# Kernel optimization log

Hardware: AMD Instinct MI355X
Metric: run time of the kernel (lower is better)

The kernel has to match this reference:

```python
import jax, jax.numpy as jnp
import numpy as np

EM_DIM = 64
GROUP = 16
DIM_IN = 1024


def _position_embedding(boxes, part_boxes):
    # boxes: [N,4], part_boxes: [P,4] -> [N,P,EM_DIM]
    xmin, ymin, xmax, ymax = [boxes[:, i:i + 1] for i in range(4)]            # [N,1]
    pxmin, pymin, pxmax, pymax = [part_boxes[:, i:i + 1].T for i in range(4)]  # [1,P]
    bw = xmax - xmin + 1.0
    bh = ymax - ymin + 1.0
    pw = pxmax - pxmin + 1.0
    ph = pymax - pymin + 1.0
    cx = 0.5 * (xmin + xmax)
    cy = 0.5 * (ymin + ymax)
    pcx = 0.5 * (pxmin + pxmax)
    pcy = 0.5 * (pymin + pymax)
    dx = jnp.abs((cx - pcx) / bw)
    dy = jnp.abs((cy - pcy) / bh)
    dx = jnp.log(jnp.where(dx < 1e-3, 1e-3, dx))
    dy = jnp.log(jnp.where(dy < 1e-3, 1e-3, dy))
    dw = jnp.log(pw / bw)
    dh = jnp.log(ph / bh)
    pos = jnp.stack([dx, dy, dw, dh], axis=2)                                  # [N,P,4]
    em_range = jnp.arange(EM_DIM // 8, dtype=pos.dtype) / (EM_DIM // 8)        # [8]
    em_mat = jnp.power(jnp.asarray(1000.0, pos.dtype), em_range)               # [8]
    div = (100.0 * pos)[..., None] / em_mat                                    # [N,P,4,8]
    emb = jnp.concatenate([jnp.sin(div), jnp.cos(div)], axis=3)                # [N,P,4,16]
    return emb.reshape(pos.shape[0], pos.shape[1], EM_DIM)


def _single_relation(boxes, part_boxes, bf, pf, Wg_w, Wg_b, Wq_w, Wq_b, Wk_w, Wk_b, conv_w, conv_b):
    N = bf.shape[0]
    P = pf.shape[0]
    emb = _position_embedding(boxes, part_boxes)                               # [N,P,64]
    pos_feat = jax.nn.relu(emb @ Wg_w.T + Wg_b)                                # [N,P,G]
    att_weight = jnp.transpose(pos_feat, (0, 2, 1))                            # [N,G,P]
    q = (bf @ Wq_w.T + Wq_b).reshape(N, GROUP, EM_DIM)                         # [N,G,64]
    k = (pf @ Wk_w.T + Wk_b).reshape(P, GROUP, EM_DIM)                         # [P,G,64]
    att = jnp.einsum('ngd,pgd->ngp', q, k) * (1.0 / GROUP)                     # [N,G,P]
    att_weight = jnp.where(att_weight < 1e-6, 1e-6, att_weight)
    sm = jax.nn.softmax(jnp.log(att_weight) + att, axis=2)                     # [N,G,P]
    out = jnp.einsum('ngp,pc->ngc', sm, pf)                                    # [N,G,dim_in]
    # grouped 1x1 conv: group g maps dim_in channels -> EM_DIM channels
    w3 = conv_w.reshape(GROUP, EM_DIM, DIM_IN)
    rel = jnp.einsum('ngc,goc->ngo', out, w3).reshape(N, GROUP * EM_DIM) + conv_b
    return rel                                                                  # [N, G*EM_DIM]


def setup_inputs() -> dict:
    key = jax.random.key(0)
    ks = jax.random.split(key, 12)
    N_TOT, P_TOT = 2048, 2048

    def make_rois(k1, k2, n, n1):
        xy = jax.random.uniform(k1, (n, 2), jnp.float32) * 800.0
        wh = jax.random.uniform(k2, (n, 2), jnp.float32) * 200.0 + 16.0
        boxes = jnp.concatenate([xy, xy + wh], axis=1)
        idx = jnp.concatenate([jnp.zeros((n1, 1)), jnp.ones((n - n1, 1))], axis=0).astype(jnp.float32)
        return jnp.concatenate([idx, boxes], axis=1)

    rois = make_rois(ks[0], ks[1], N_TOT, 1024)
    part_rois = make_rois(ks[2], ks[3], P_TOT, 1024)
    box_feats = jax.random.normal(ks[4], (N_TOT, DIM_IN), jnp.float32)
    part_feats = jax.random.normal(ks[5], (P_TOT, DIM_IN), jnp.float32)
    xav_g = float(np.sqrt(6.0 / (EM_DIM + GROUP)))
    xav_qk = float(np.sqrt(6.0 / (DIM_IN + GROUP * EM_DIM)))
    Wg_w = jax.random.uniform(ks[6], (GROUP, EM_DIM), jnp.float32, -xav_g, xav_g)
    Wg_b = jnp.zeros((GROUP,), jnp.float32)
    Wq_w = jax.random.uniform(ks[7], (GROUP * EM_DIM, DIM_IN), jnp.float32, -xav_qk, xav_qk)
    Wq_b = jnp.zeros((GROUP * EM_DIM,), jnp.float32)
    Wk_w = jax.random.uniform(ks[8], (GROUP * EM_DIM, DIM_IN), jnp.float32, -xav_qk, xav_qk)
    Wk_b = jnp.zeros((GROUP * EM_DIM,), jnp.float32)
    conv_w = jax.random.normal(ks[9], (GROUP * EM_DIM, DIM_IN), jnp.float32) * 0.02
    conv_b = jnp.zeros((GROUP * EM_DIM,), jnp.float32)
    return {"rois": rois, "part_rois": part_rois, "box_feats": box_feats,
            "part_feats": part_feats, "Wg_w": Wg_w, "Wg_b": Wg_b,
            "Wq_w": Wq_w, "Wq_b": Wq_b, "Wk_w": Wk_w, "Wk_b": Wk_b,
            "conv_w": conv_w, "conv_b": conv_b, "n1_boxes": 1024, "n1_parts": 1024}


def reference(rois, part_rois, box_feats, part_feats, Wg_w, Wg_b, Wq_w, Wq_b,
              Wk_w, Wk_b, conv_w, conv_b, n1_boxes, n1_parts):
    boxes = rois[:, 1:5]
    part_boxes = part_rois[:, 1:5]
    params = (Wg_w, Wg_b, Wq_w, Wq_b, Wk_w, Wk_b, conv_w, conv_b)
    rel1 = _single_relation(boxes[:n1_boxes], part_boxes[:n1_parts],
                            box_feats[:n1_boxes], part_feats[:n1_parts], *params)
    rel2 = _single_relation(boxes[n1_boxes:], part_boxes[n1_parts:],
                            box_feats[n1_boxes:], part_feats[n1_parts:], *params)
    return jnp.concatenate([rel1, rel2], axis=0)  # [N_total, GROUP*EM_DIM]
```

## Files before the change

kernel.cpp:

```cpp
#include <hip/hip_runtime.h>

typedef unsigned short u16;
using short8  = __attribute__((ext_vector_type(8))) short;
using float4v = __attribute__((ext_vector_type(4))) float;

__device__ __forceinline__ u16 f2bf(float f) {
    union { float f; unsigned u; } v; v.f = f;
    unsigned r = (v.u + 0x7fff + ((v.u >> 16) & 1)) >> 16;
    return (u16)r;
}
__device__ __forceinline__ float bf2f(u16 h) {
    union { unsigned u; float f; } v; v.u = ((unsigned)h) << 16; return v.f;
}
__device__ __forceinline__ unsigned pkbf(float lo, float hi) {
    unsigned d;
    asm("v_cvt_pk_bf16_f32 %0, %1, %2" : "=v"(d) : "v"(lo), "v"(hi));
    return d;
}
__device__ __forceinline__ float sin_rev(float r) {
    float f, s;
    asm("v_fract_f32 %0, %1" : "=v"(f) : "v"(r));
    asm("v_sin_f32 %0, %1" : "=v"(s) : "v"(f));
    return s;
}
__device__ __forceinline__ void dma16(const void* g, void* l) {
    __builtin_amdgcn_global_load_lds((const __attribute__((address_space(1))) void*)g,
                                     (__attribute__((address_space(3))) void*)l, 16, 0, 0);
}

__device__ __forceinline__ void cvt4(const float* __restrict__ s, u16* __restrict__ o, int i) {
    float4 v = ((const float4*)s)[i];
    uint2 r; r.x = pkbf(v.x, v.y); r.y = pkbf(v.z, v.w);
    ((uint2*)o)[i] = r;
}

__global__ __launch_bounds__(256)
void cvt_all(const float* __restrict__ s0, const float* __restrict__ s1,
             const float* __restrict__ s2, const float* __restrict__ s3,
             const float* __restrict__ s4, const float* __restrict__ prois,
             u16* __restrict__ o0, u16* __restrict__ o1, u16* __restrict__ o2,
             u16* __restrict__ o3, u16* __restrict__ o4, float4* __restrict__ PD,
             int na4, int nb4, int nw4, int PT) {
    int i = blockIdx.x * 256 + threadIdx.x;
    if (i < na4) { cvt4(s0, o0, i); return; }
    i -= na4;
    if (i < nb4) { cvt4(s1, o1, i); return; }
    i -= nb4;
    if (i < nw4) { cvt4(s2, o2, i); return; }
    i -= nw4;
    if (i < nw4) { cvt4(s3, o3, i); return; }
    i -= nw4;
    if (i < nw4) { cvt4(s4, o4, i); return; }
    i -= nw4;
    if (i < PT) {
        const float* pr = prois + (size_t)i * 5;
        float pxmin = pr[1], pymin = pr[2], pxmax = pr[3], pymax = pr[4];
        PD[i] = make_float4(0.5f * (pxmin + pxmax), 0.5f * (pymin + pymax),
                            __logf(pxmax - pxmin + 1.0f), __logf(pymax - pymin + 1.0f));
    }
}

__global__ __launch_bounds__(256)
void proj_posw(const u16* __restrict__ Ab, const u16* __restrict__ Pb,
               const u16* __restrict__ Wqb, const u16* __restrict__ Wkb,
               const u16* __restrict__ Cwb, const float* __restrict__ bq,
               const float* __restrict__ bk, u16* __restrict__ Qb,
               u16* __restrict__ Kb, u16* __restrict__ PVt,
               const float* __restrict__ rois, const float4* __restrict__ PD,
               const float* __restrict__ Wg_w, const float* __restrict__ Wg_b,
               u16* __restrict__ POSW, const int* __restrict__ n1b_p,
               const int* __restrict__ n1p_p, int PT) {
    __shared__ __align__(16) u16 SH[20992];

    const int grp = blockIdx.x / 11, rem = blockIdx.x % 11;
    const int t = threadIdx.x;
    const int w = t >> 6, lane = t & 63;
    const int fm = lane & 15, quad = lane >> 4;

    if (rem < 3) {
        u16* As = SH;
        u16* Ws = SH + 8192;
        u16* Tr = SH + 12288;
        const int pb = grp * 3 + rem;
        const int z = pb >> 8;
        const int m0 = ((pb >> 4) & 15) * 128, j0 = (pb & 15) * 64;
        const u16* A = (z == 0) ? Ab : Pb;
        const u16* W = (z == 0) ? Wqb : (z == 1 ? Wkb : Cwb);
        const int wm = w >> 1, wn = w & 1;
        const int lr = lane >> 3, lc = lane & 7, gch = lc ^ lr;

        float4v zero4 = {0.f, 0.f, 0.f, 0.f};
        float4v acc[4][2];
#pragma unroll
        for (int i = 0; i < 4; ++i) { acc[i][0] = zero4; acc[i][1] = zero4; }

        for (int k0 = 0; k0 < 1024; k0 += 64) {
#pragma unroll
            for (int i = 0; i < 4; ++i) {
                int row = w * 32 + i * 8 + lr;
                dma16(A + (size_t)(m0 + row) * 1024 + k0 + gch * 8,
                      As + (w * 32 + i * 8) * 64 + lane * 8);
            }
#pragma unroll
            for (int i = 0; i < 2; ++i) {
                int row = w * 16 + i * 8 + lr;
                dma16(W + (size_t)(j0 + row) * 1024 + k0 + gch * 8,
                      Ws + (w * 16 + i * 8) * 64 + lane * 8);
            }
            __syncthreads();
#pragma unroll
            for (int ks = 0; ks < 2; ++ks) {
                int c = ks * 4 + quad;
                short8 af[4], bf[2];
#pragma unroll
                for (int i = 0; i < 4; ++i) {
                    int ra = wm * 64 + i * 16 + fm;
                    af[i] = *(const short8*)(As + ra * 64 + ((c ^ (ra & 7)) * 8));
                }
#pragma unroll
                for (int j = 0; j < 2; ++j) {
                    int rb = wn * 32 + j * 16 + fm;
                    bf[j] = *(const short8*)(Ws + rb * 64 + ((c ^ (rb & 7)) * 8));
                }
#pragma unroll
                for (int i = 0; i < 4; ++i)
#pragma unroll
                    for (int j = 0; j < 2; ++j)
                        acc[i][j] = __builtin_amdgcn_mfma_f32_16x16x32_bf16(af[i], bf[j], acc[i][j], 0, 0, 0);
            }
            __syncthreads();
        }

        if (z < 2) {
            u16* O = z ? Kb : Qb;
            const float* bias = z ? bk : bq;
#pragma unroll
            for (int j = 0; j < 2; ++j) {
                int jl = wn * 32 + j * 16 + fm;
                float bb = bias[j0 + jl];
#pragma unroll
                for (int i = 0; i < 4; ++i) {
                    int mlb = wm * 64 + i * 16 + quad * 4;
#pragma unroll
                    for (int r = 0; r < 4; ++r)
                        Tr[(mlb + r) * 68 + jl] = f2bf(acc[i][j][r] + bb);
                }
            }
            __syncthreads();
#pragma unroll
            for (int i2 = 0; i2 < 4; ++i2) {
                int f = i2 * 2048 + t * 8;
                int ml = f >> 6, jl = f & 63;
                union { uint2 u2[2]; short8 s8; } uu;
                uu.u2[0] = *(const uint2*)(Tr + ml * 68 + jl);
                uu.u2[1] = *(const uint2*)(Tr + ml * 68 + jl + 4);
                *(short8*)(O + (size_t)(m0 + ml) * 1024 + j0 + jl) = uu.s8;
            }
        } else {
#pragma unroll
            for (int j = 0; j < 2; ++j) {
                int jl = wn * 32 + j * 16 + fm;
#pragma unroll
                for (int i = 0; i < 4; ++i) {
                    int mlb = wm * 64 + i * 16 + quad * 4;
                    uint2 pk;
                    pk.x = pkbf(acc[i][j][0], acc[i][j][1]);
                    pk.y = pkbf(acc[i][j][2], acc[i][j][3]);
                    *(uint2*)(Tr + jl * 136 + mlb) = pk;
                }
            }
            __syncthreads();
#pragma unroll
            for (int i2 = 0; i2 < 4; ++i2) {
                int f = i2 * 2048 + t * 8;
                int jl = f >> 7, ml = f & 127;
                union { uint2 u2[2]; short8 s8; } uu;
                uu.u2[0] = *(const uint2*)(Tr + jl * 136 + ml);
                uu.u2[1] = *(const uint2*)(Tr + jl * 136 + ml + 4);
                *(short8*)(PVt + (size_t)(j0 + jl) * PT + m0 + ml) = uu.s8;
            }
        }
        return;
    }

    u16* Wl = SH + w * 4224;

    const int n = grp * 8 + (rem - 3);
    const int n1b = *n1b_p, n1p = *n1p_p;
    const int hh = (n >= n1b) ? 1 : 0;
    const int p0 = hh ? n1p : 0;
    const int Ph = hh ? (PT - n1p) : n1p;

    float xmin = rois[n * 5 + 1], ymin = rois[n * 5 + 2];
    float xmax = rois[n * 5 + 3], ymax = rois[n * 5 + 4];
    float bw = xmax - xmin + 1.0f, bh = ymax - ymin + 1.0f;
    float cx = 0.5f * (xmin + xmax), cy = 0.5f * (ymin + ymax);

    const int jA = quad >> 1, trig = quad & 1;
    float cA   = (jA == 0) ? cx : cy;
    float invA = (jA == 0) ? (1.0f / bw) : (1.0f / bh);
    float lB   = (jA == 0) ? __logf(bw) : __logf(bh);
    float toff = trig ? 0.25f : 0.0f;

    const int g_ = fm;
    short8 b1, b2;
    {
        const float* w1 = Wg_w + g_ * 64 + quad * 8;
        const float* w2 = Wg_w + g_ * 64 + 32 + quad * 8;
        unsigned* p1 = (unsigned*)&b1;
        unsigned* p2 = (unsigned*)&b2;
#pragma unroll
        for (int kk = 0; kk < 4; ++kk) {
            p1[kk] = pkbf(w1[2 * kk], w1[2 * kk + 1]);
            p2[kk] = pkbf(w2[2 * kk], w2[2 * kk + 1]);
        }
    }
    float wgb = Wg_b[g_];

    const float inv_em[8] = {1.0f, 0.4216965034f, 0.1778279410f, 0.0749894209f,
                             0.0316227766f, 0.0133352143f, 0.0056234133f, 0.0023713737f};
    const float REV = 15.91549431f;
    const int prange = Ph >> 2;
    const int pb0 = w * prange;

    float4 pd_c = PD[p0 + pb0 + fm];

#pragma unroll 2
    for (int pt = 0; pt < 16; ++pt) {
        float4 pd_n;
        if (pt < 15) pd_n = PD[p0 + pb0 + pt * 16 + 16 + fm];
        float pc = (jA == 0) ? pd_c.x : pd_c.y;
        float lp = (jA == 0) ? pd_c.z : pd_c.w;
        float posA = __logf(fmaxf(fabsf(cA - pc) * invA, 0.001f));
        float posB = lp - lB;
        float br1 = posA * REV, br2 = posB * REV;
        float e1[8], e2[8];
#pragma unroll
        for (int k = 0; k < 8; ++k) {
            e1[k] = sin_rev(fmaf(br1, inv_em[k], toff));
            e2[k] = sin_rev(fmaf(br2, inv_em[k], toff));
        }
        short8 a1, a2;
        unsigned* pa1 = (unsigned*)&a1;
        unsigned* pa2 = (unsigned*)&a2;
#pragma unroll
        for (int kk = 0; kk < 4; ++kk) {
            pa1[kk] = pkbf(e1[2 * kk], e1[2 * kk + 1]);
            pa2[kk] = pkbf(e2[2 * kk], e2[2 * kk + 1]);
        }
        float4v acc = {wgb, wgb, wgb, wgb};
        acc = __builtin_amdgcn_mfma_f32_16x16x32_bf16(a1, b1, acc, 0, 0, 0);
        acc = __builtin_amdgcn_mfma_f32_16x16x32_bf16(a2, b2, acc, 0, 0, 0);

        float w0  = fmaxf(acc[0], 1e-6f);
        float w1v = fmaxf(acc[1], 1e-6f);
        float w2v = fmaxf(acc[2], 1e-6f);
        float w3v = fmaxf(acc[3], 1e-6f);
        uint2 wp; wp.x = pkbf(w0, w1v); wp.y = pkbf(w2v, w3v);
        *(uint2*)(Wl + pt * 264 + lane * 4) = wp;

        pd_c = pd_n;
    }

    const int p8 = (lane & 31) * 8;
    const int halfg = lane >> 5;
    const int itq = p8 >> 4;
    const int q0 = (p8 >> 2) & 3;
#pragma unroll
    for (int s = 0; s < 8; ++s) {
        int gg = s * 2 + halfg;
        union { uint2 u2[2]; short8 s8; } uu;
        uu.u2[0] = *(const uint2*)(Wl + itq * 264 + (q0 * 16 + gg) * 4);
        uu.u2[1] = *(const uint2*)(Wl + itq * 264 + ((q0 + 1) * 16 + gg) * 4);
        *(short8*)(POSW + ((size_t)n * 16 + gg) * 1024 + pb0 + p8) = uu.s8;
    }
}

__global__ __launch_bounds__(256)
void fused_rel(const u16* __restrict__ Qb, const u16* __restrict__ Kb,
               const u16* __restrict__ POSW, const u16* __restrict__ PVt,
               const float* __restrict__ conv_b, float* __restrict__ OUT,
               const int* __restrict__ n1b_p, const int* __restrict__ n1p_p, int PT) {
    __shared__ __align__(16) u16 Qs[64 * 64];
    __shared__ __align__(16) u16 Ks[2][64 * 64];
    __shared__ __align__(16) u16 Ps[2][64 * 64];
    __shared__ __align__(16) u16 Vs[2][64 * 64];
    __shared__ __align__(16) u16 Wt[4][16 * 64];

    const int n0 = blockIdx.x * 64, g = blockIdx.y;
    const int n1b = *n1b_p, n1p = *n1p_p;
    const int hh = (n0 >= n1b) ? 1 : 0;
    const int p0 = hh ? n1p : 0;
    const int Ph = hh ? (PT - n1p) : n1p;
    const int t = threadIdx.x;
    const int w = t >> 6, lane = t & 63;
    const int lr = lane >> 3, lc = lane & 7, gch = lc ^ lr;
    const int fm = lane & 15, quad = lane >> 4;
    const int swz = fm & 7;

    auto stage = [&](int pt, int buf) {
#pragma unroll
        for (int i = 0; i < 2; ++i) {
            int row = w * 16 + i * 8 + lr;
            dma16(Kb + (size_t)(p0 + pt * 64 + row) * 1024 + g * 64 + gch * 8,
                  Ks[buf] + (w * 16 + i * 8) * 64 + lane * 8);
            dma16(POSW + ((size_t)(n0 + row) * 16 + g) * 1024 + pt * 64 + gch * 8,
                  Ps[buf] + (w * 16 + i * 8) * 64 + lane * 8);
            dma16(PVt + (size_t)(g * 64 + row) * PT + p0 + pt * 64 + gch * 8,
                  Vs[buf] + (w * 16 + i * 8) * 64 + lane * 8);
        }
    };

    stage(0, 0);
#pragma unroll
    for (int i = 0; i < 2; ++i) {
        int row = w * 16 + i * 8 + lr;
        dma16(Qb + (size_t)(n0 + row) * 1024 + g * 64 + gch * 8,
              Qs + (w * 16 + i * 8) * 64 + lane * 8);
    }

    float4v zero4 = {0.f, 0.f, 0.f, 0.f};
    float4v oacc[4];
#pragma unroll
    for (int ob = 0; ob < 4; ++ob) oacc[ob] = zero4;
    float rsum = 0.0f;

    __syncthreads();

    const int nloc = w * 16 + fm;
    short8 qf[2];
#pragma unroll
    for (int kd = 0; kd < 2; ++kd) {
        int c = kd * 4 + quad;
        qf[kd] = *(const short8*)(Qs + nloc * 64 + ((c ^ swz) * 8));
    }
    u16* wrow = Wt[w] + fm * 64;

    const int NPT = Ph >> 6;
    for (int pt = 0; pt < NPT; ++pt) {
        int cur = pt & 1;
        if (pt + 1 < NPT) stage(pt + 1, cur ^ 1);
        const u16* ks_ = Ks[cur];
        const u16* ps_ = Ps[cur];
        const u16* vs_ = Vs[cur];

        float4v atc[4];
#pragma unroll
        for (int pi = 0; pi < 4; ++pi) atc[pi] = zero4;
#pragma unroll
        for (int kd = 0; kd < 2; ++kd) {
            int c = kd * 4 + quad;
#pragma unroll
            for (int pi = 0; pi < 4; ++pi) {
                int rp = pi * 16 + fm;
                short8 kf = *(const short8*)(ks_ + rp * 64 + ((c ^ swz) * 8));
                atc[pi] = __builtin_amdgcn_mfma_f32_16x16x32_bf16(kf, qf[kd], atc[pi], 0, 0, 0);
            }
        }

#pragma unroll
        for (int pi = 0; pi < 4; ++pi) {
            int co = ((pi * 2 + (quad >> 1)) ^ swz) * 8 + (quad & 1) * 4;
            uint2 pwp = *(const uint2*)(ps_ + nloc * 64 + co);
            const u16* pww = (const u16*)&pwp;
            float wv0 = bf2f(pww[0]) * __expf(atc[pi][0] * 0.0625f);
            float wv1 = bf2f(pww[1]) * __expf(atc[pi][1] * 0.0625f);
            float wv2 = bf2f(pww[2]) * __expf(atc[pi][2] * 0.0625f);
            float wv3 = bf2f(pww[3]) * __expf(atc[pi][3] * 0.0625f);
            rsum += (wv0 + wv1) + (wv2 + wv3);
            uint2 wp; wp.x = pkbf(wv0, wv1); wp.y = pkbf(wv2, wv3);
            *(uint2*)(wrow + co) = wp;
        }

#pragma unroll
        for (int m = 0; m < 2; ++m) {
            short8 af = *(const short8*)(wrow + (((m * 4 + quad) ^ swz) * 8));
#pragma unroll
            for (int ob = 0; ob < 4; ++ob) {
                int ro = ob * 16 + fm;
                short8 vf = *(const short8*)(vs_ + ro * 64 + (((m * 4 + quad) ^ swz) * 8));
                oacc[ob] = __builtin_amdgcn_mfma_f32_16x16x32_bf16(af, vf, oacc[ob], 0, 0, 0);
            }
        }

        __syncthreads();
    }

    float s = rsum;
    s += __shfl_xor(s, 16, 64);
    s += __shfl_xor(s, 32, 64);
    float inv[4];
#pragma unroll
    for (int r = 0; r < 4; ++r)
        inv[r] = 1.0f / __shfl(s, quad * 4 + r, 64);

    float bb[4];
#pragma unroll
    for (int ob = 0; ob < 4; ++ob) bb[ob] = conv_b[g * 64 + ob * 16 + fm];
#pragma unroll
    for (int ob = 0; ob < 4; ++ob)
#pragma unroll
        for (int r = 0; r < 4; ++r) {
            int nn = n0 + w * 16 + quad * 4 + r;
            OUT[(size_t)nn * 1024 + g * 64 + ob * 16 + fm] = oacc[ob][r] * inv[r] + bb[ob];
        }
}

extern "C" void kernel_launch(void* const* d_in, const int* in_sizes, int n_in,
                              void* d_out, int out_size, void* d_ws, size_t ws_size,
                              hipStream_t stream) {
    const float* rois   = (const float*)d_in[0];
    const float* prois  = (const float*)d_in[1];
    const float* bfeat  = (const float*)d_in[2];
    const float* pfeat  = (const float*)d_in[3];
    const float* Wg_w   = (const float*)d_in[4];
    const float* Wg_b   = (const float*)d_in[5];
    const float* Wq_w   = (const float*)d_in[6];
    const float* Wq_b   = (const float*)d_in[7];
    const float* Wk_w   = (const float*)d_in[8];
    const float* Wk_b   = (const float*)d_in[9];
    const float* conv_w = (const float*)d_in[10];
    const float* conv_b = (const float*)d_in[11];
    const int*   n1b    = (const int*)d_in[12];
    const int*   n1p    = (const int*)d_in[13];

    const int NT = in_sizes[2] / 1024;
    const int PT = in_sizes[3] / 1024;

    u16* Qb   = (u16*)d_ws;
    u16* Kb   = Qb + (size_t)NT * 1024;
    u16* PVt  = Kb + (size_t)PT * 1024;
    float4* PD = (float4*)(PVt + (size_t)1024 * PT);
    u16* POSW = (u16*)(PD + PT);
    u16* Ab   = POSW + (size_t)NT * 16 * 1024;
    u16* Pb   = Ab + (size_t)NT * 1024;
    u16* Wqb  = Pb + (size_t)PT * 1024;
    u16* Wkb  = Wqb + 1024 * 1024;
    u16* Cwb  = Wkb + 1024 * 1024;

    dim3 blk(256);
    int nf4 = NT * 1024 / 4, pf4 = PT * 1024 / 4, wf4 = 1024 * 1024 / 4;
    int tot = nf4 + pf4 + 3 * wf4 + PT;
    cvt_all<<<dim3((tot + 255) / 256), blk, 0, stream>>>(
        bfeat, pfeat, Wq_w, Wk_w, conv_w, prois, Ab, Pb, Wqb, Wkb, Cwb, PD,
        nf4, pf4, wf4, PT);

    proj_posw<<<dim3(256 * 11), blk, 0, stream>>>(Ab, Pb, Wqb, Wkb, Cwb,
                                                  Wq_b, Wk_b, Qb, Kb, PVt,
                                                  rois, PD, Wg_w, Wg_b, POSW,
                                                  n1b, n1p, PT);
    fused_rel<<<dim3(NT / 64, 16), blk, 0, stream>>>(Qb, Kb, POSW, PVt, conv_b,
                                                     (float*)d_out, n1b, n1p, PT);
}
```

Before: 173.8 us.

## Precompute part-box sin/cos tables and use angle-subtraction for width/height embedding

The dw/dh embedding term, log(pw)-log(bw), is separable. The per-part sin/cos of log(pw) are now computed once per part in the conversion kernel and stored in a table. Each pos-weight block combines them with per-box sin/cos through the angle-difference identity, replacing 8 hardware sin evaluations per iteration with table loads and FMAs. The pos-weight tile is also staged in two halves, which roughly halves shared memory (the GEMM transpose buffer now aliases the A buffer) to allow more resident blocks. The cost is extra global reads of the trig table and a small change in numerics.

```diff
diff --git a/kernel.cpp b/kernel.cpp
--- a/kernel.cpp
+++ b/kernel.cpp
@@ -27,6 +27,8 @@
     __builtin_amdgcn_global_load_lds((const __attribute__((address_space(1))) void*)g,
                                      (__attribute__((address_space(3))) void*)l, 16, 0, 0);
 }
+
+#define REVC 15.91549431f
 
 __device__ __forceinline__ void cvt4(const float* __restrict__ s, u16* __restrict__ o, int i) {
     float4 v = ((const float4*)s)[i];
@@ -40,7 +42,7 @@
              const float* __restrict__ s4, const float* __restrict__ prois,
              u16* __restrict__ o0, u16* __restrict__ o1, u16* __restrict__ o2,
              u16* __restrict__ o3, u16* __restrict__ o4, float4* __restrict__ PD,
-             int na4, int nb4, int nw4, int PT) {
+             float* __restrict__ PTRIG, int na4, int nb4, int nw4, int PT) {
     int i = blockIdx.x * 256 + threadIdx.x;
     if (i < na4) { cvt4(s0, o0, i); return; }
     i -= na4;
@@ -53,10 +55,22 @@
     if (i < nw4) { cvt4(s4, o4, i); return; }
     i -= nw4;
     if (i < PT) {
+        const float inv_em[8] = {1.0f, 0.4216965034f, 0.1778279410f, 0.0749894209f,
+                                 0.0316227766f, 0.0133352143f, 0.0056234133f, 0.0023713737f};
         const float* pr = prois + (size_t)i * 5;
         float pxmin = pr[1], pymin = pr[2], pxmax = pr[3], pymax = pr[4];
-        PD[i] = make_float4(0.5f * (pxmin + pxmax), 0.5f * (pymin + pymax),
-                            __logf(pxmax - pxmin + 1.0f), __logf(pymax - pymin + 1.0f));
+        float lpw = __logf(pxmax - pxmin + 1.0f), lph = __logf(pymax - pymin + 1.0f);
+        PD[i] = make_float4(0.5f * (pxmin + pxmax), 0.5f * (pymin + pymax), lpw, lph);
+        float* tp = PTRIG + (size_t)i * 32;
+        float aw = lpw * REVC, ah = lph * REVC;
+#pragma unroll
+        for (int k = 0; k < 8; ++k) {
+            float a = aw * inv_em[k], b = ah * inv_em[k];
+            tp[k]      = sin_rev(a);
+            tp[8 + k]  = sin_rev(a + 0.25f);
+            tp[16 + k] = sin_rev(b);
+            tp[24 + k] = sin_rev(b + 0.25f);
+        }
     }
 }
 
@@ -67,10 +81,11 @@
                const float* __restrict__ bk, u16* __restrict__ Qb,
                u16* __restrict__ Kb, u16* __restrict__ PVt,
                const float* __restrict__ rois, const float4* __restrict__ PD,
+               const float* __restrict__ PTRIG,
                const float* __restrict__ Wg_w, const float* __restrict__ Wg_b,
                u16* __restrict__ POSW, const int* __restrict__ n1b_p,
                const int* __restrict__ n1p_p, int PT) {
-    __shared__ __align__(16) u16 SH[20992];
+    __shared__ __align__(16) u16 SH[12288];
 
     const int grp = blockIdx.x / 11, rem = blockIdx.x % 11;
     const int t = threadIdx.x;
@@ -80,7 +95,7 @@
     if (rem < 3) {
         u16* As = SH;
         u16* Ws = SH + 8192;
-        u16* Tr = SH + 12288;
+        u16* Tr = SH;
         const int pb = grp * 3 + rem;
         const int z = pb >> 8;
         const int m0 = ((pb >> 4) & 15) * 128, j0 = (pb & 15) * 64;
@@ -183,7 +198,7 @@
         return;
     }
 
-    u16* Wl = SH + w * 4224;
+    u16* Wl = SH + w * 2112;
 
     const int n = grp * 8 + (rem - 3);
     const int n1b = *n1b_p, n1p = *n1p_p;
@@ -201,6 +216,23 @@
     float invA = (jA == 0) ? (1.0f / bw) : (1.0f / bh);
     float lB   = (jA == 0) ? __logf(bw) : __logf(bh);
     float toff = trig ? 0.25f : 0.0f;
+
+    const float inv_em[8] = {1.0f, 0.4216965034f, 0.1778279410f, 0.0749894209f,
+                             0.0316227766f, 0.0133352143f, 0.0056234133f, 0.0023713737f};
+
+    float cb[8], sbx[8];
+    {
+        float sgn = trig ? 1.0f : -1.0f;
+        float bn = lB * REVC;
+#pragma unroll
+        for (int k = 0; k < 8; ++k) {
+            float b = bn * inv_em[k];
+            cb[k]  = sin_rev(b + 0.25f);
+            sbx[k] = sgn * sin_rev(b);
+        }
+    }
+    const float* TU = PTRIG + jA * 16 + trig * 8;
+    const float* TV = PTRIG + jA * 16 + (1 - trig) * 8;
 
     const int g_ = fm;
     short8 b1, b2;
@@ -217,62 +249,75 @@
     }
     float wgb = Wg_b[g_];
 
-    const float inv_em[8] = {1.0f, 0.4216965034f, 0.1778279410f, 0.0749894209f,
-                             0.0316227766f, 0.0133352143f, 0.0056234133f, 0.0023713737f};
-    const float REV = 15.91549431f;
     const int prange = Ph >> 2;
     const int pb0 = w * prange;
 
     float4 pd_c = PD[p0 + pb0 + fm];
 
+    for (int half = 0; half < 2; ++half) {
 #pragma unroll 2
-    for (int pt = 0; pt < 16; ++pt) {
-        float4 pd_n;
-        if (pt < 15) pd_n = PD[p0 + pb0 + pt * 16 + 16 + fm];
-        float pc = (jA == 0) ? pd_c.x : pd_c.y;
-        float lp = (jA == 0) ? pd_c.z : pd_c.w;
-        float posA = __logf(fmaxf(fabsf(cA - pc) * invA, 0.001f));
-        float posB = lp - lB;
-        float br1 = posA * REV, br2 = posB * REV;
-        float e1[8], e2[8];
-#pragma unroll
-        for (int k = 0; k < 8; ++k) {
-            e1[k] = sin_rev(fmaf(br1, inv_em[k], toff));
-            e2[k] = sin_rev(fmaf(br2, inv_em[k], toff));
-        }
-        short8 a1, a2;
-        unsigned* pa1 = (unsigned*)&a1;
-        unsigned* pa2 = (unsigned*)&a2;
-#pragma unroll
-        for (int kk = 0; kk < 4; ++kk) {
-            pa1[kk] = pkbf(e1[2 * kk], e1[2 * kk + 1]);
-            pa2[kk] = pkbf(e2[2 * kk], e2[2 * kk + 1]);
-        }
-        float4v acc = {wgb, wgb, wgb, wgb};
-        acc = __builtin_amdgcn_mfma_f32_16x16x32_bf16(a1, b1, acc, 0, 0, 0);
-        acc = __builtin_amdgcn_mfma_f32_16x16x32_bf16(a2, b2, acc, 0, 0, 0);
-
-        float w0  = fmaxf(acc[0], 1e-6f);
-        float w1v = fmaxf(acc[1], 1e-6f);
-        float w2v = fmaxf(acc[2], 1e-6f);
-        float w3v = fmaxf(acc[3], 1e-6f);
-        uint2 wp; wp.x = pkbf(w0, w1v); wp.y = pkbf(w2v, w3v);
-        *(uint2*)(Wl + pt * 264 + lane * 4) = wp;
-
-        pd_c = pd_n;
-    }
-
-    const int p8 = (lane & 31) * 8;
-    const int halfg = lane >> 5;
-    const int itq = p8 >> 4;
-    const int q0 = (p8 >> 2) & 3;
-#pragma unroll
-    for (int s = 0; s < 8; ++s) {
-        int gg = s * 2 + halfg;
-        union { uint2 u2[2]; short8 s8; } uu;
-        uu.u2[0] = *(const uint2*)(Wl + itq * 264 + (q0 * 16 + gg) * 4);
-        uu.u2[1] = *(const uint2*)(Wl + itq * 264 + ((q0 + 1) * 16 + gg) * 4);
-        *(short8*)(POSW + ((size_t)n * 16 + gg) * 1024 + pb0 + p8) = uu.s8;
+        for (int pt8 = 0; pt8 < 8; ++pt8) {
+            int pt = half * 8 + pt8;
+            int pp = p0 + pb0 + pt * 16 + fm;
+            float4 pd_n;
+            if (pt < 15) pd_n = PD[pp + 16];
+
+            float pc = (jA == 0) ? pd_c.x : pd_c.y;
+            float posA = __logf(fmaxf(fabsf(cA - pc) * invA, 0.001f));
+            float br1 = posA * REVC;
+            float e1[8];
+#pragma unroll
+            for (int k = 0; k < 8; ++k)
+                e1[k] = sin_rev(fmaf(br1, inv_em[k], toff));
+
+            const float* tu = TU + (size_t)pp * 32;
+            const float* tv = TV + (size_t)pp * 32;
+            float4 U0 = *(const float4*)tu, U1 = *(const float4*)(tu + 4);
+            float4 V0 = *(const float4*)tv, V1 = *(const float4*)(tv + 4);
+            float e2[8];
+            e2[0] = fmaf(U0.x, cb[0], V0.x * sbx[0]);
+            e2[1] = fmaf(U0.y, cb[1], V0.y * sbx[1]);
+            e2[2] = fmaf(U0.z, cb[2], V0.z * sbx[2]);
+            e2[3] = fmaf(U0.w, cb[3], V0.w * sbx[3]);
+            e2[4] = fmaf(U1.x, cb[4], V1.x * sbx[4]);
+            e2[5] = fmaf(U1.y, cb[5], V1.y * sbx[5]);
+            e2[6] = fmaf(U1.z, cb[6], V1.z * sbx[6]);
+            e2[7] = fmaf(U1.w, cb[7], V1.w * sbx[7]);
+
+            short8 a1, a2;
+            unsigned* pa1 = (unsigned*)&a1;
+            unsigned* pa2 = (unsigned*)&a2;
+#pragma unroll
+            for (int kk = 0; kk < 4; ++kk) {
+                pa1[kk] = pkbf(e1[2 * kk], e1[2 * kk + 1]);
+                pa2[kk] = pkbf(e2[2 * kk], e2[2 * kk + 1]);
+            }
+            float4v acc = {wgb, wgb, wgb, wgb};
+            acc = __builtin_amdgcn_mfma_f32_16x16x32_bf16(a1, b1, acc, 0, 0, 0);
+            acc = __builtin_amdgcn_mfma_f32_16x16x32_bf16(a2, b2, acc, 0, 0, 0);
+
+            float w0  = fmaxf(acc[0], 1e-6f);
+            float w1v = fmaxf(acc[1], 1e-6f);
+            float w2v = fmaxf(acc[2], 1e-6f);
+            float w3v = fmaxf(acc[3], 1e-6f);
+            uint2 wp; wp.x = pkbf(w0, w1v); wp.y = pkbf(w2v, w3v);
+            *(uint2*)(Wl + pt8 * 264 + lane * 4) = wp;
+
+            pd_c = pd_n;
+        }
+        {
+            const int p8 = (lane & 15) * 8;
+            const int itq = p8 >> 4, q0 = (p8 >> 2) & 3;
+            const int phh = half * 128;
+#pragma unroll
+            for (int s = 0; s < 4; ++s) {
+                int gg = s * 4 + (lane >> 4);
+                union { uint2 u2[2]; short8 s8; } uu;
+                uu.u2[0] = *(const uint2*)(Wl + itq * 264 + (q0 * 16 + gg) * 4);
+                uu.u2[1] = *(const uint2*)(Wl + itq * 264 + ((q0 + 1) * 16 + gg) * 4);
+                *(short8*)(POSW + ((size_t)n * 16 + gg) * 1024 + pb0 + phh + p8) = uu.s8;
+            }
+        }
     }
 }
 
@@ -431,7 +476,8 @@
     u16* Kb   = Qb + (size_t)NT * 1024;
     u16* PVt  = Kb + (size_t)PT * 1024;
     float4* PD = (float4*)(PVt + (size_t)1024 * PT);
-    u16* POSW = (u16*)(PD + PT);
+    float* PTRIG = (float*)(PD + PT);
+    u16* POSW = (u16*)(PTRIG + (size_t)PT * 32);
     u16* Ab   = POSW + (size_t)NT * 16 * 1024;
     u16* Pb   = Ab + (size_t)NT * 1024;
     u16* Wqb  = Pb + (size_t)PT * 1024;
@@ -443,11 +489,11 @@
     int tot = nf4 + pf4 + 3 * wf4 + PT;
     cvt_all<<<dim3((tot + 255) / 256), blk, 0, stream>>>(
         bfeat, pfeat, Wq_w, Wk_w, conv_w, prois, Ab, Pb, Wqb, Wkb, Cwb, PD,
-        nf4, pf4, wf4, PT);
+        PTRIG, nf4, pf4, wf4, PT);
 
     proj_posw<<<dim3(256 * 11), blk, 0, stream>>>(Ab, Pb, Wqb, Wkb, Cwb,
                                                   Wq_b, Wk_b, Qb, Kb, PVt,
-                                                  rois, PD, Wg_w, Wg_b, POSW,
+                                                  rois, PD, PTRIG, Wg_w, Wg_b, POSW,
                                                   n1b, n1p, PT);
     fused_rel<<<dim3(NT / 64, 16), blk, 0, stream>>>(Qb, Kb, POSW, PVt, conv_b,
                                                      (float*)d_out, n1b, n1p, PT);
```

New measurement: 214.3 us. 23.3% more time.

## Replace async LDS DMA staging with register prefetch and deeper POSW lookahead

Applied to the files above, without the earlier changes.

The attention kernel stops using direct global-to-LDS dma16 loads for K, V and POSW tiles. It now loads the next tile into registers at the top of each iteration, writes them to the other LDS buffer after the MFMA work, and prefetches POSW two tiles ahead. The projection kernel also overlaps its transpose scratch with the A tile buffer to cut shared memory, which could raise occupancy. The trade is higher register pressure and extra LDS write instructions in the loop.

```diff
diff --git a/kernel.cpp b/kernel.cpp
--- a/kernel.cpp
+++ b/kernel.cpp
@@ -70,7 +70,7 @@
                const float* __restrict__ Wg_w, const float* __restrict__ Wg_b,
                u16* __restrict__ POSW, const int* __restrict__ n1b_p,
                const int* __restrict__ n1p_p, int PT) {
-    __shared__ __align__(16) u16 SH[20992];
+    __shared__ __align__(16) u16 SH[16896];
 
     const int grp = blockIdx.x / 11, rem = blockIdx.x % 11;
     const int t = threadIdx.x;
@@ -80,7 +80,7 @@
     if (rem < 3) {
         u16* As = SH;
         u16* Ws = SH + 8192;
-        u16* Tr = SH + 12288;
+        u16* Tr = SH;
         const int pb = grp * 3 + rem;
         const int z = pb >> 8;
         const int m0 = ((pb >> 4) & 15) * 128, j0 = (pb & 15) * 64;
@@ -298,26 +298,28 @@
     const int fm = lane & 15, quad = lane >> 4;
     const int swz = fm & 7;
 
-    auto stage = [&](int pt, int buf) {
-#pragma unroll
-        for (int i = 0; i < 2; ++i) {
-            int row = w * 16 + i * 8 + lr;
-            dma16(Kb + (size_t)(p0 + pt * 64 + row) * 1024 + g * 64 + gch * 8,
-                  Ks[buf] + (w * 16 + i * 8) * 64 + lane * 8);
-            dma16(POSW + ((size_t)(n0 + row) * 16 + g) * 1024 + pt * 64 + gch * 8,
-                  Ps[buf] + (w * 16 + i * 8) * 64 + lane * 8);
-            dma16(PVt + (size_t)(g * 64 + row) * PT + p0 + pt * 64 + gch * 8,
-                  Vs[buf] + (w * 16 + i * 8) * 64 + lane * 8);
-        }
-    };
-
-    stage(0, 0);
-#pragma unroll
-    for (int i = 0; i < 2; ++i) {
-        int row = w * 16 + i * 8 + lr;
-        dma16(Qb + (size_t)(n0 + row) * 1024 + g * 64 + gch * 8,
-              Qs + (w * 16 + i * 8) * 64 + lane * 8);
-    }
+    const int row0 = w * 16 + lr, row1 = w * 16 + 8 + lr;
+    const size_t kb0 = (size_t)(p0 + row0) * 1024 + g * 64 + gch * 8;
+    const size_t kb1 = (size_t)(p0 + row1) * 1024 + g * 64 + gch * 8;
+    const size_t vb0 = (size_t)(g * 64 + row0) * PT + p0 + gch * 8;
+    const size_t vb1 = (size_t)(g * 64 + row1) * PT + p0 + gch * 8;
+    const size_t pbs0 = ((size_t)(n0 + row0) * 16 + g) * 1024 + gch * 8;
+    const size_t pbs1 = ((size_t)(n0 + row1) * 16 + g) * 1024 + gch * 8;
+    const int d0 = (w * 16) * 64 + lane * 8;
+    const int d1 = (w * 16 + 8) * 64 + lane * 8;
+
+    dma16(Qb + (size_t)(n0 + row0) * 1024 + g * 64 + gch * 8, Qs + d0);
+    dma16(Qb + (size_t)(n0 + row1) * 1024 + g * 64 + gch * 8, Qs + d1);
+    {
+        uint4 ka = *(const uint4*)(Kb + kb0), kbv = *(const uint4*)(Kb + kb1);
+        uint4 va = *(const uint4*)(PVt + vb0), vb = *(const uint4*)(PVt + vb1);
+        uint4 pa = *(const uint4*)(POSW + pbs0), pbv = *(const uint4*)(POSW + pbs1);
+        *(uint4*)(Ks[0] + d0) = ka;  *(uint4*)(Ks[0] + d1) = kbv;
+        *(uint4*)(Vs[0] + d0) = va;  *(uint4*)(Vs[0] + d1) = vb;
+        *(uint4*)(Ps[0] + d0) = pa;  *(uint4*)(Ps[0] + d1) = pbv;
+    }
+    uint4 prH0 = *(const uint4*)(POSW + pbs0 + 64);
+    uint4 prH1 = *(const uint4*)(POSW + pbs1 + 64);
 
     float4v zero4 = {0.f, 0.f, 0.f, 0.f};
     float4v oacc[4];
@@ -338,11 +340,24 @@
 
     const int NPT = Ph >> 6;
     for (int pt = 0; pt < NPT; ++pt) {
-        int cur = pt & 1;
-        if (pt + 1 < NPT) stage(pt + 1, cur ^ 1);
+        const int cur = pt & 1, nxt = cur ^ 1;
         const u16* ks_ = Ks[cur];
         const u16* ps_ = Ps[cur];
         const u16* vs_ = Vs[cur];
+        const bool have1 = (pt + 1 < NPT), have2 = (pt + 2 < NPT);
+
+        uint4 kra, krb, vra, vrb, prN0, prN1;
+        if (have1) {
+            size_t o = (size_t)(pt + 1) * 65536;
+            kra = *(const uint4*)(Kb + kb0 + o);
+            krb = *(const uint4*)(Kb + kb1 + o);
+            vra = *(const uint4*)(PVt + vb0 + (pt + 1) * 64);
+            vrb = *(const uint4*)(PVt + vb1 + (pt + 1) * 64);
+        }
+        if (have2) {
+            prN0 = *(const uint4*)(POSW + pbs0 + (pt + 2) * 64);
+            prN1 = *(const uint4*)(POSW + pbs1 + (pt + 2) * 64);
+        }
 
         float4v atc[4];
 #pragma unroll
@@ -381,6 +396,13 @@
                 short8 vf = *(const short8*)(vs_ + ro * 64 + (((m * 4 + quad) ^ swz) * 8));
                 oacc[ob] = __builtin_amdgcn_mfma_f32_16x16x32_bf16(af, vf, oacc[ob], 0, 0, 0);
             }
+        }
+
+        if (have1) {
+            *(uint4*)(Ks[nxt] + d0) = kra;  *(uint4*)(Ks[nxt] + d1) = krb;
+            *(uint4*)(Vs[nxt] + d0) = vra;  *(uint4*)(Vs[nxt] + d1) = vrb;
+            *(uint4*)(Ps[nxt] + d0) = prH0; *(uint4*)(Ps[nxt] + d1) = prH1;
+            prH0 = prN0; prH1 = prN1;
         }
 
         __syncthreads();
```

Result: faster. 168.8 us, median of 3 (-2.9%).
